# Optimization experiments

Measured on AMD Instinct MI355X. Metric: run time of the kernel, lower is better.

Reference implementation:

```python
import jax, jax.numpy as jnp
import numpy as np

B, S, A, H, NH = 4, 4096, 512, 1024, 16
HD = H // NH  # 64


def setup_inputs() -> dict:
    key = jax.random.key(0)
    ks = jax.random.split(key, 12)
    s = 1.0 / np.sqrt(H)
    return {
        "hidden_states": jax.random.normal(ks[0], (B, S, H), jnp.float32),
        "audio_tokens": jax.random.normal(ks[1], (B, A, H), jnp.float32),
        "attention_mask": jax.random.randint(ks[2], (B, A), 0, 2, jnp.int32),
        "Wq": jax.random.normal(ks[3], (H, H), jnp.float32) * s,
        "bq": jnp.zeros((H,), jnp.float32),
        "Wk": jax.random.normal(ks[4], (H, H), jnp.float32) * s,
        "bk": jnp.zeros((H,), jnp.float32),
        "Wv": jax.random.normal(ks[5], (H, H), jnp.float32) * s,
        "bv": jnp.zeros((H,), jnp.float32),
        "Wo": jax.random.normal(ks[6], (H, H), jnp.float32) * s,
        "bo": jnp.zeros((H,), jnp.float32),
        "ln_gamma": jnp.ones((H,), jnp.float32),
        "ln_beta": jnp.zeros((H,), jnp.float32),
        "residual_scale": jnp.asarray(0.05, jnp.float32),
    }


def _san(x, big=10000.0):
    return jnp.nan_to_num(x, nan=0.0, posinf=big, neginf=-big)


def reference(hidden_states, audio_tokens, attention_mask, Wq, bq, Wk, bk, Wv, bv,
              Wo, bo, ln_gamma, ln_beta, residual_scale):
    hs = _san(hidden_states).astype(jnp.float32)
    at = _san(audio_tokens).astype(jnp.float32)

    def heads(x, W, b):  # [b, t, H] -> [b, t, nh, hd]
        return _san(x @ W.T + b).reshape(x.shape[0], x.shape[1], NH, HD)

    q = heads(hs, Wq, bq)            # [B,S,NH,HD]
    k = heads(at, Wk, bk)            # [B,A,NH,HD]
    v = heads(at, Wv, bv)            # [B,A,NH,HD]

    scale = max(np.sqrt(HD), 1e-8)
    scores = jnp.einsum("bsnd,band->bnsa", q, k) / scale  # [B,NH,S,A]
    scores = jnp.clip(_san(jnp.clip(scores, -50.0, 50.0), 50.0), -50.0, 50.0)

    attend = (attention_mask > 0)[:, None, None, :]       # [B,1,1,A]
    scores = jnp.where(attend, scores, -10000.0)
    scores = jnp.clip(scores, -50.0, 50.0)

    probs = jax.nn.softmax(scores, axis=-1)
    probs = _san(probs, 1.0)
    probs = probs / (jnp.sum(probs, axis=-1, keepdims=True) + 1e-8)

    ctx = jnp.einsum("bnsa,band->bsnd", probs, v).reshape(B, S, H)
    delta = _san(ctx @ Wo.T + bo)

    rs = jnp.clip(residual_scale, 0.0, 0.3)
    delta = rs * delta

    mu = jnp.mean(delta, axis=-1, keepdims=True)
    var = jnp.mean(jnp.square(delta - mu), axis=-1, keepdims=True)
    delta = (delta - mu) / jnp.sqrt(var + 1e-5) * ln_gamma + ln_beta
    return delta
```

## Files before the change

kernel.cpp:

```cpp
#include <hip/hip_runtime.h>
#include <hip/hip_bf16.h>
#include <cstdint>
#include <cstddef>

#define B_  4
#define S_  4096
#define A_  512
#define H_  1024
#define NH_ 16
#define HD_ 64

typedef __bf16 bf16;
typedef __bf16 bf16x8 __attribute__((ext_vector_type(8)));
typedef __bf16 bf16x4 __attribute__((ext_vector_type(4)));
typedef float  fx4    __attribute__((ext_vector_type(4)));

typedef __attribute__((address_space(3))) void LDS_v;
typedef const __attribute__((address_space(1))) void GLB_v;

__device__ __forceinline__ void gl_lds16(const void* g, void* l) {
    __builtin_amdgcn_global_load_lds((GLB_v*)g, (LDS_v*)l, 16, 0, 0);
}

__device__ __forceinline__ float sanf(float x) {
    if (x != x) return 0.f;
    if (fabsf(x) == __builtin_inff()) return x > 0.f ? 10000.f : -10000.f;
    return x;
}

__global__ __launch_bounds__(256) void cast_all(const float* __restrict__ hs,
                                                const float* __restrict__ at,
                                                const float* __restrict__ wq,
                                                const float* __restrict__ wk,
                                                const float* __restrict__ wv,
                                                const float* __restrict__ wo,
                                                bf16* __restrict__ dhs, bf16* __restrict__ dat,
                                                bf16* __restrict__ dwq, bf16* __restrict__ dwk,
                                                bf16* __restrict__ dwv, bf16* __restrict__ dwo) {
    int i = blockIdx.x * 256 + threadIdx.x;
    const float* s; bf16* d; int off;
    if (i < 4194304)      { s = hs; d = dhs; off = i; }
    else if (i < 4718592) { s = at; d = dat; off = i - 4194304; }
    else if (i < 4980736) { s = wq; d = dwq; off = i - 4718592; }
    else if (i < 5242880) { s = wk; d = dwk; off = i - 4980736; }
    else if (i < 5505024) { s = wv; d = dwv; off = i - 5242880; }
    else                  { s = wo; d = dwo; off = i - 5505024; }
    float4 v = ((const float4*)s)[off];
    bf16x4 o;
    o[0] = (bf16)sanf(v.x); o[1] = (bf16)sanf(v.y);
    o[2] = (bf16)sanf(v.z); o[3] = (bf16)sanf(v.w);
    *(bf16x4*)&d[(size_t)off * 4] = o;
}

__global__ __launch_bounds__(256) void qkv_gemm(const bf16* __restrict__ hsb,
                                                const bf16* __restrict__ atb,
                                                const bf16* __restrict__ wqb,
                                                const bf16* __restrict__ wkb,
                                                const bf16* __restrict__ wvb,
                                                const float* __restrict__ bq,
                                                const float* __restrict__ bk,
                                                const float* __restrict__ bv,
                                                bf16* __restrict__ Qb,
                                                bf16* __restrict__ Kb,
                                                bf16* __restrict__ Vtb) {
    __shared__ __align__(16) bf16 As[128 * 32];
    __shared__ __align__(16) bf16 Bs[128 * 32];

    const int id = blockIdx.x;
    int mode, m0, n0;
    const bf16 *A, *Bt; const float* bias;
    if (id < 1024)      { mode = 0; m0 = (id & 127) * 128; n0 = (id >> 7) * 128; A = hsb; Bt = wqb; bias = bq; }
    else if (id < 1152) { int t = id - 1024; mode = 1; m0 = (t & 15) * 128; n0 = (t >> 4) * 128; A = atb; Bt = wkb; bias = bk; }
    else                { int t = id - 1152; mode = 2; m0 = (t & 15) * 128; n0 = (t >> 4) * 128; A = atb; Bt = wvb; bias = bv; }

    const int tid  = threadIdx.x;
    const int lane = tid & 63;
    const int wv   = tid >> 6;
    const int wr   = wv >> 1, wc = wv & 1;
    const int lr   = lane & 15, kq = lane >> 4;

    fx4 acc[4][4] = {};

    const bf16* Ag = A  + (size_t)m0 * 1024;
    const bf16* Bg = Bt + (size_t)n0 * 1024;
    const int c0 = tid, c1 = tid + 256;
    const int row0 = c0 >> 2, kc0 = c0 & 3;
    const int row1 = c1 >> 2, kc1 = c1 & 3;

    for (int k0 = 0; k0 < 1024; k0 += 32) {
        gl_lds16(Ag + (size_t)row0 * 1024 + k0 + kc0 * 8, &As[c0 * 8]);
        gl_lds16(Ag + (size_t)row1 * 1024 + k0 + kc1 * 8, &As[c1 * 8]);
        gl_lds16(Bg + (size_t)row0 * 1024 + k0 + kc0 * 8, &Bs[c0 * 8]);
        gl_lds16(Bg + (size_t)row1 * 1024 + k0 + kc1 * 8, &Bs[c1 * 8]);
        __syncthreads();
        bf16x8 af[4], bfr[4];
#pragma unroll
        for (int i = 0; i < 4; i++) af[i]  = *(const bf16x8*)&As[(wr * 64 + i * 16 + lr) * 32 + kq * 8];
#pragma unroll
        for (int j = 0; j < 4; j++) bfr[j] = *(const bf16x8*)&Bs[(wc * 64 + j * 16 + lr) * 32 + kq * 8];
#pragma unroll
        for (int i = 0; i < 4; i++)
#pragma unroll
            for (int j = 0; j < 4; j++)
                acc[i][j] = __builtin_amdgcn_mfma_f32_16x16x32_bf16(af[i], bfr[j], acc[i][j], 0, 0, 0);
        __syncthreads();
    }

    float bb[4];
#pragma unroll
    for (int j = 0; j < 4; j++) bb[j] = bias[n0 + wc * 64 + j * 16 + lr];

    if (mode == 0) {
        const float sc = 0.18033688011112042f;
#pragma unroll
        for (int i = 0; i < 4; i++) {
            int row = m0 + wr * 64 + i * 16 + kq * 4;
#pragma unroll
            for (int j = 0; j < 4; j++) {
                int col = n0 + wc * 64 + j * 16 + lr;
#pragma unroll
                for (int r = 0; r < 4; r++)
                    Qb[(size_t)(row + r) * 1024 + col] = (bf16)((acc[i][j][r] + bb[j]) * sc);
            }
        }
    } else if (mode == 1) {
#pragma unroll
        for (int i = 0; i < 4; i++) {
            int row = m0 + wr * 64 + i * 16 + kq * 4;
#pragma unroll
            for (int j = 0; j < 4; j++) {
                int col = n0 + wc * 64 + j * 16 + lr;
#pragma unroll
                for (int r = 0; r < 4; r++)
                    Kb[(size_t)(row + r) * 1024 + col] = (bf16)(acc[i][j][r] + bb[j]);
            }
        }
    } else {
#pragma unroll
        for (int i = 0; i < 4; i++) {
            int m = m0 + wr * 64 + i * 16 + kq * 4;
            int bidx = m >> 9, a = m & 511;
#pragma unroll
            for (int j = 0; j < 4; j++) {
                int col = n0 + wc * 64 + j * 16 + lr;
                bf16x4 o;
#pragma unroll
                for (int r = 0; r < 4; r++) o[r] = (bf16)(acc[i][j][r] + bb[j]);
                *(bf16x4*)&Vtb[((size_t)bidx * H_ + col) * A_ + a] = o;
            }
        }
    }
}

__global__ __launch_bounds__(256) void gemm_o(const bf16* __restrict__ A,
                                              const bf16* __restrict__ Bt,
                                              const float* __restrict__ bias,
                                              bf16* __restrict__ C,
                                              const float* __restrict__ rsp) {
    __shared__ __align__(16) bf16 As[128 * 32];
    __shared__ __align__(16) bf16 Bs[128 * 32];

    const int tid  = threadIdx.x;
    const int lane = tid & 63;
    const int wv   = tid >> 6;
    const int wr   = wv >> 1, wc = wv & 1;
    const int lr   = lane & 15, kq = lane >> 4;
    const int m0   = blockIdx.x * 128, n0 = blockIdx.y * 128;

    fx4 acc[4][4] = {};

    const bf16* Ag = A  + (size_t)m0 * 1024;
    const bf16* Bg = Bt + (size_t)n0 * 1024;
    const int c0 = tid, c1 = tid + 256;
    const int row0 = c0 >> 2, kc0 = c0 & 3;
    const int row1 = c1 >> 2, kc1 = c1 & 3;

    for (int k0 = 0; k0 < 1024; k0 += 32) {
        gl_lds16(Ag + (size_t)row0 * 1024 + k0 + kc0 * 8, &As[c0 * 8]);
        gl_lds16(Ag + (size_t)row1 * 1024 + k0 + kc1 * 8, &As[c1 * 8]);
        gl_lds16(Bg + (size_t)row0 * 1024 + k0 + kc0 * 8, &Bs[c0 * 8]);
        gl_lds16(Bg + (size_t)row1 * 1024 + k0 + kc1 * 8, &Bs[c1 * 8]);
        __syncthreads();
        bf16x8 af[4], bfr[4];
#pragma unroll
        for (int i = 0; i < 4; i++) af[i]  = *(const bf16x8*)&As[(wr * 64 + i * 16 + lr) * 32 + kq * 8];
#pragma unroll
        for (int j = 0; j < 4; j++) bfr[j] = *(const bf16x8*)&Bs[(wc * 64 + j * 16 + lr) * 32 + kq * 8];
#pragma unroll
        for (int i = 0; i < 4; i++)
#pragma unroll
            for (int j = 0; j < 4; j++)
                acc[i][j] = __builtin_amdgcn_mfma_f32_16x16x32_bf16(af[i], bfr[j], acc[i][j], 0, 0, 0);
        __syncthreads();
    }

    float bb[4];
#pragma unroll
    for (int j = 0; j < 4; j++) bb[j] = bias[n0 + wc * 64 + j * 16 + lr];
    float rs = fminf(fmaxf(rsp[0], 0.f), 0.3f);
#pragma unroll
    for (int i = 0; i < 4; i++) {
        int row = m0 + wr * 64 + i * 16 + kq * 4;
#pragma unroll
        for (int j = 0; j < 4; j++) {
            int col = n0 + wc * 64 + j * 16 + lr;
#pragma unroll
            for (int r = 0; r < 4; r++)
                C[(size_t)(row + r) * 1024 + col] = (bf16)(rs * (acc[i][j][r] + bb[j]));
        }
    }
}

__global__ __launch_bounds__(256, 4) void attn_kernel(const bf16* __restrict__ Q,
                                                      const bf16* __restrict__ Kb,
                                                      const bf16* __restrict__ Vt,
                                                      const int* __restrict__ mask,
                                                      bf16* __restrict__ ctx) {
    __shared__ __align__(16) bf16 Qs[128 * 72];
    __shared__ __align__(16) bf16 Ks[64 * 72];
    __shared__ __align__(16) bf16 Vts[64 * 72];
    __shared__ float smask[512];

    const int tid  = threadIdx.x;
    const int lane = tid & 63;
    const int wv   = tid >> 6;
    const int lr   = lane & 15, kq = lane >> 4;
    const int st = blockIdx.x, h = blockIdx.y, b = blockIdx.z;
    const int m0 = b * S_ + st * 128;
    const float LO = -72.134752f;

    bf16x8 qtmp[4];
#pragma unroll
    for (int i = 0; i < 4; i++) {
        int c = tid + i * 256, row = c >> 3, ch = c & 7;
        qtmp[i] = *(const bf16x8*)(Q + (size_t)(m0 + row) * H_ + h * 64 + ch * 8);
    }
    smask[tid]       = (mask[b * A_ + tid] > 0)       ? -LO : LO;
    smask[tid + 256] = (mask[b * A_ + tid + 256] > 0) ? -LO : LO;
#pragma unroll
    for (int i = 0; i < 4; i++) {
        int c = tid + i * 256, row = c >> 3, ch = c & 7;
        *(bf16x8*)&Qs[row * 72 + ch * 8] = qtmp[i];
    }

    const int srow = tid >> 2, sseg = tid & 3;
    const size_t kg = (size_t)(b * A_ + srow) * H_ + h * 64 + sseg * 16;
    const bf16* vrow = Vt + (size_t)(b * H_ + h * 64 + srow) * A_;
    const int va0 = 32 * (sseg >> 1) + 4 * ((2 * sseg) & 3);
    const int va1 = 32 * (sseg >> 1) + 4 * ((2 * sseg + 1) & 3);

    bf16x8 kr0 = *(const bf16x8*)(Kb + kg);
    bf16x8 kr1 = *(const bf16x8*)(Kb + kg + 8);
    bf16x4 v00 = *(const bf16x4*)(vrow + va0);
    bf16x4 v01 = *(const bf16x4*)(vrow + va0 + 16);
    bf16x4 v10 = *(const bf16x4*)(vrow + va1);
    bf16x4 v11 = *(const bf16x4*)(vrow + va1 + 16);

    fx4 acco[2][4] = {};
    fx4 accd[2] = {};

    bf16x8 vone;
#pragma unroll
    for (int e = 0; e < 8; e++) vone[e] = (bf16)1.0f;

    for (int it = 0; it < 8; it++) {
        const int a0 = it * 64;
        __syncthreads();
        *(bf16x8*)&Ks[srow * 72 + sseg * 16]      = kr0;
        *(bf16x8*)&Ks[srow * 72 + sseg * 16 + 8]  = kr1;
        *(bf16x8*)&Vts[srow * 72 + sseg * 16] =
            __builtin_shufflevector(v00, v01, 0, 1, 2, 3, 4, 5, 6, 7);
        *(bf16x8*)&Vts[srow * 72 + sseg * 16 + 8] =
            __builtin_shufflevector(v10, v11, 0, 1, 2, 3, 4, 5, 6, 7);
        __syncthreads();

        if (it < 7) {
            const size_t ko = kg + (size_t)(a0 + 64) * H_;
            kr0 = *(const bf16x8*)(Kb + ko);
            kr1 = *(const bf16x8*)(Kb + ko + 8);
            v00 = *(const bf16x4*)(vrow + a0 + 64 + va0);
            v01 = *(const bf16x4*)(vrow + a0 + 64 + va0 + 16);
            v10 = *(const bf16x4*)(vrow + a0 + 64 + va1);
            v11 = *(const bf16x4*)(vrow + a0 + 64 + va1 + 16);
        }

        fx4 accs[4][2] = {};
#pragma unroll
        for (int kk = 0; kk < 64; kk += 32) {
            bf16x8 kf[4], qf[2];
#pragma unroll
            for (int mt = 0; mt < 4; mt++)
                kf[mt] = *(const bf16x8*)&Ks[(mt * 16 + lr) * 72 + kk + kq * 8];
#pragma unroll
            for (int nt = 0; nt < 2; nt++)
                qf[nt] = *(const bf16x8*)&Qs[(wv * 32 + nt * 16 + lr) * 72 + kk + kq * 8];
#pragma unroll
            for (int mt = 0; mt < 4; mt++)
#pragma unroll
                for (int nt = 0; nt < 2; nt++)
                    accs[mt][nt] = __builtin_amdgcn_mfma_f32_16x16x32_bf16(kf[mt], qf[nt], accs[mt][nt], 0, 0, 0);
        }

        bf16x8 pa[2][2];
#pragma unroll
        for (int mt = 0; mt < 4; mt++) {
            fx4 cap = *(const fx4*)&smask[a0 + mt * 16 + kq * 4];
#pragma unroll
            for (int nt = 0; nt < 2; nt++) {
#pragma unroll
                for (int r = 0; r < 4; r++) {
                    float p = __builtin_amdgcn_exp2f(fminf(accs[mt][nt][r], cap[r]));
                    pa[mt >> 1][nt][(mt & 1) * 4 + r] = (bf16)p;
                }
            }
        }

#pragma unroll
        for (int ks = 0; ks < 2; ks++) {
#pragma unroll
            for (int stl = 0; stl < 2; stl++)
                accd[stl] = __builtin_amdgcn_mfma_f32_16x16x32_bf16(pa[ks][stl], vone, accd[stl], 0, 0, 0);
#pragma unroll
            for (int dt = 0; dt < 4; dt++) {
                bf16x8 vf = *(const bf16x8*)&Vts[(dt * 16 + lr) * 72 + ks * 32 + kq * 8];
#pragma unroll
                for (int stl = 0; stl < 2; stl++)
                    acco[stl][dt] = __builtin_amdgcn_mfma_f32_16x16x32_bf16(pa[ks][stl], vf, acco[stl][dt], 0, 0, 0);
            }
        }
    }

#pragma unroll
    for (int stl = 0; stl < 2; stl++) {
        float ri[4];
#pragma unroll
        for (int r = 0; r < 4; r++) ri[r] = __builtin_amdgcn_rcpf(accd[stl][r]);
#pragma unroll
        for (int dt = 0; dt < 4; dt++)
#pragma unroll
            for (int r = 0; r < 4; r++)
                Qs[(wv * 32 + stl * 16 + kq * 4 + r) * 72 + dt * 16 + lr] =
                    (bf16)(acco[stl][dt][r] * ri[r]);
    }
    __syncthreads();
#pragma unroll
    for (int i = 0; i < 4; i++) {
        int c = tid + i * 256, row = c >> 3, ch = c & 7;
        *(bf16x8*)&ctx[(size_t)(m0 + row) * H_ + h * 64 + ch * 8] = *(const bf16x8*)&Qs[row * 72 + ch * 8];
    }
}

__global__ __launch_bounds__(256) void ln_kernel(const bf16* __restrict__ in,
                                                 float* __restrict__ out,
                                                 const float* __restrict__ gamma,
                                                 const float* __restrict__ beta) {
    __shared__ float red[8];
    const int tid = threadIdx.x;
    bf16x4 xb = *(const bf16x4*)&in[(size_t)blockIdx.x * 1024 + tid * 4];
    float x0 = (float)xb[0], x1 = (float)xb[1], x2 = (float)xb[2], x3 = (float)xb[3];
    float s = x0 + x1 + x2 + x3;
    float q = x0 * x0 + x1 * x1 + x2 * x2 + x3 * x3;
#pragma unroll
    for (int off = 32; off > 0; off >>= 1) {
        s += __shfl_down(s, off);
        q += __shfl_down(q, off);
    }
    if ((tid & 63) == 0) { red[(tid >> 6) * 2] = s; red[(tid >> 6) * 2 + 1] = q; }
    __syncthreads();
    s = red[0] + red[2] + red[4] + red[6];
    q = red[1] + red[3] + red[5] + red[7];
    float mean = s * (1.f / 1024.f);
    float var  = q * (1.f / 1024.f) - mean * mean;
    float inv  = rsqrtf(var + 1e-5f);
    float4 g  = ((const float4*)gamma)[tid];
    float4 bb = ((const float4*)beta)[tid];
    float4 y;
    y.x = (x0 - mean) * inv * g.x + bb.x;
    y.y = (x1 - mean) * inv * g.y + bb.y;
    y.z = (x2 - mean) * inv * g.z + bb.z;
    y.w = (x3 - mean) * inv * g.w + bb.w;
    ((float4*)(out + (size_t)blockIdx.x * 1024))[tid] = y;
}

extern "C" void kernel_launch(void* const* d_in, const int* in_sizes, int n_in,
                              void* d_out, int out_size, void* d_ws, size_t ws_size,
                              hipStream_t stream) {
    const float* hs    = (const float*)d_in[0];
    const float* at    = (const float*)d_in[1];
    const int*   maskp = (const int*)d_in[2];
    const float* Wq    = (const float*)d_in[3];
    const float* bq    = (const float*)d_in[4];
    const float* Wk    = (const float*)d_in[5];
    const float* bk    = (const float*)d_in[6];
    const float* Wv    = (const float*)d_in[7];
    const float* bv    = (const float*)d_in[8];
    const float* Wo    = (const float*)d_in[9];
    const float* bo    = (const float*)d_in[10];
    const float* gamma = (const float*)d_in[11];
    const float* beta  = (const float*)d_in[12];
    const float* rsp   = (const float*)d_in[13];

    char* ws = (char*)d_ws;
    bf16* hsb = (bf16*)(ws + 0);
    bf16* ctx = (bf16*)(ws + 0);
    bf16* atb = (bf16*)(ws + 33554432);
    bf16* wqb = (bf16*)(ws + 37748736);
    bf16* wkb = (bf16*)(ws + 39845888);
    bf16* wvb = (bf16*)(ws + 41943040);
    bf16* wob = (bf16*)(ws + 44040192);
    bf16* Qb  = (bf16*)(ws + 46137344);
    bf16* Ob  = Qb;
    bf16* Kb  = (bf16*)(ws + 79691776);
    bf16* Vtb = (bf16*)(ws + 83886080);

    cast_all<<<22528, 256, 0, stream>>>(hs, at, Wq, Wk, Wv, Wo,
                                        hsb, atb, wqb, wkb, wvb, wob);

    qkv_gemm<<<1280, 256, 0, stream>>>(hsb, atb, wqb, wkb, wvb,
                                       bq, bk, bv, Qb, Kb, Vtb);

    attn_kernel<<<dim3(32, 16, 4), 256, 0, stream>>>(Qb, Kb, Vtb, maskp, ctx);

    gemm_o<<<dim3(128, 8), 256, 0, stream>>>(ctx, wob, bo, Ob, rsp);
    ln_kernel<<<16384, 256, 0, stream>>>(Ob, (float*)d_out, gamma, beta);
}
```

Baseline: 322.6 us.

## Rewrite projection GEMMs as 256x256 double-buffered pipelined tiles with XCD-aware remapping

Replaces the 128x128 QKV and output-projection GEMMs with 512-thread 256x256-tile kernels. These use double-buffered LDS, direct global-to-LDS loads, an XOR swizzle against bank conflicts, s_setprio around the MFMA bursts, and explicit waitcnt/barrier pipelining. Block indices are remapped so neighbouring tiles land on the same XCD, and the same remap is applied to the attention and layernorm grids. Attention now keeps Q fragments in registers instead of staging them through LDS. The aim is more data reuse per tile and better L2 locality, at the cost of higher register and LDS pressure and fewer blocks in flight.

```diff
diff --git a/kernel.cpp b/kernel.cpp
--- a/kernel.cpp
+++ b/kernel.cpp
@@ -52,164 +52,217 @@
     *(bf16x4*)&d[(size_t)off * 4] = o;
 }
 
-__global__ __launch_bounds__(256) void qkv_gemm(const bf16* __restrict__ hsb,
-                                                const bf16* __restrict__ atb,
-                                                const bf16* __restrict__ wqb,
-                                                const bf16* __restrict__ wkb,
-                                                const bf16* __restrict__ wvb,
-                                                const float* __restrict__ bq,
-                                                const float* __restrict__ bk,
-                                                const float* __restrict__ bv,
-                                                bf16* __restrict__ Qb,
-                                                bf16* __restrict__ Kb,
-                                                bf16* __restrict__ Vtb) {
-    __shared__ __align__(16) bf16 As[128 * 32];
-    __shared__ __align__(16) bf16 Bs[128 * 32];
+
+#define GEMM_PRO()                                                                     \
+    STG(0, 0, 0, 0); STG(1, 0, 0, 0); STG(0, 1, 0, 0); STG(1, 1, 0, 0);                \
+    asm volatile("s_waitcnt vmcnt(4)" ::: "memory");                                   \
+    __builtin_amdgcn_s_barrier();
+
+#define GEMM_PH(ACC0_, ACCOFF_, KS_, BI_, STGM_, STGH_, KN_, SI_, DOVM_)               \
+    {                                                                                  \
+        if (ACC0_) {                                                                   \
+            for (int j2 = 0; j2 < 4; j2++) bfr[j2] = DSRB(j2, KS_, BI_);               \
+        }                                                                              \
+        for (int i = 0; i < 4; i++) af[i] = DSRA(i + ACCOFF_, KS_, BI_);               \
+        STG(STGM_, STGH_, KN_, SI_);                                                   \
+        __builtin_amdgcn_s_barrier();                                                  \
+        asm volatile("s_waitcnt lgkmcnt(0)" ::: "memory");                             \
+        __builtin_amdgcn_s_setprio(1);                                                 \
+        for (int i = 0; i < 4; i++)                                                    \
+            for (int j2 = 0; j2 < 4; j2++)                                             \
+                acc[i + ACCOFF_][j2] = __builtin_amdgcn_mfma_f32_16x16x32_bf16(        \
+                    af[i], bfr[j2], acc[i + ACCOFF_][j2], 0, 0, 0);                    \
+        __builtin_amdgcn_s_setprio(0);                                                 \
+        if (DOVM_) { asm volatile("s_waitcnt vmcnt(4)" ::: "memory"); }                \
+        __builtin_amdgcn_s_barrier();                                                  \
+    }
+
+#define GEMM_BODY()                                                                    \
+    fx4 acc[8][4] = {};                                                                \
+    GEMM_PRO();                                                                        \
+    for (int kt = 0; kt < 15; ++kt) {                                                  \
+        const int bi = kt & 1, si = bi ^ 1, kn = kt + 1;                               \
+        bf16x8 af[4], bfr[4];                                                          \
+        GEMM_PH(1, 0, 0, bi, 0, 0, kn, si, 0)                                 \
+        GEMM_PH(0, 4, 0, bi, 1, 0, kn, si, 1)                      \
+        GEMM_PH(1, 0, 1, bi, 0, 1, kn, si, 0)                                 \
+        GEMM_PH(0, 4, 1, bi, 1, 1, kn, si, 1)                      \
+    }                                                                                  \
+    {                                         \
+        const int bi = 1;                                                              \
+        bf16x8 af[4], bfr[4];                                                          \
+        for (int j2 = 0; j2 < 4; j2++) bfr[j2] = DSRB(j2, 0, bi);                      \
+        for (int i = 0; i < 4; i++) af[i] = DSRA(i, 0, bi);                            \
+        __builtin_amdgcn_s_setprio(1);                                                 \
+        for (int i = 0; i < 4; i++)                                                    \
+            for (int j2 = 0; j2 < 4; j2++)                                             \
+                acc[i][j2] = __builtin_amdgcn_mfma_f32_16x16x32_bf16(af[i], bfr[j2], acc[i][j2], 0, 0, 0); \
+        __builtin_amdgcn_s_setprio(0);                                                 \
+        for (int i = 0; i < 4; i++) af[i] = DSRA(i + 4, 0, bi);                        \
+        __builtin_amdgcn_s_setprio(1);                                                 \
+        for (int i = 0; i < 4; i++)                                                    \
+            for (int j2 = 0; j2 < 4; j2++)                                             \
+                acc[i + 4][j2] = __builtin_amdgcn_mfma_f32_16x16x32_bf16(af[i], bfr[j2], acc[i + 4][j2], 0, 0, 0); \
+        __builtin_amdgcn_s_setprio(0);                                                 \
+        asm volatile("s_waitcnt vmcnt(0)" ::: "memory");                               \
+        __builtin_amdgcn_s_barrier();                                                  \
+        for (int j2 = 0; j2 < 4; j2++) bfr[j2] = DSRB(j2, 1, bi);                      \
+        for (int i = 0; i < 4; i++) af[i] = DSRA(i, 1, bi);                            \
+        __builtin_amdgcn_s_setprio(1);                                                 \
+        for (int i = 0; i < 4; i++)                                                    \
+            for (int j2 = 0; j2 < 4; j2++)                                             \
+                acc[i][j2] = __builtin_amdgcn_mfma_f32_16x16x32_bf16(af[i], bfr[j2], acc[i][j2], 0, 0, 0); \
+        __builtin_amdgcn_s_setprio(0);                                                 \
+        for (int i = 0; i < 4; i++) af[i] = DSRA(i + 4, 1, bi);                        \
+        __builtin_amdgcn_s_setprio(1);                                                 \
+        for (int i = 0; i < 4; i++)                                                    \
+            for (int j2 = 0; j2 < 4; j2++)                                             \
+                acc[i + 4][j2] = __builtin_amdgcn_mfma_f32_16x16x32_bf16(af[i], bfr[j2], acc[i + 4][j2], 0, 0, 0); \
+        __builtin_amdgcn_s_setprio(0);                                                 \
+    }
+
+#define GEMM_COMMON_DECLS()                                                            \
+    const int tid  = threadIdx.x;                                                      \
+    const int lane = tid & 63;                                                         \
+    const int w8   = tid >> 6;                                                         \
+    const int wm   = w8 >> 2, wn = w8 & 3;                                             \
+    const int lr   = lane & 15, kq = lane >> 4;                                        \
+    const int swz  = (((lr >> 1) & 1) << 4) | (((lr >> 2) & 1) << 3);                  \
+    const int g = lane ^ (((lane >> 3) & 1) << 1) ^ ((lane >> 4) & 1);
+
+#define STG(MS_, kh_, kt_, si_) do {                                                   \
+        const bf16* s_ = (MS_ ? Bsrc : Asrc) + (kt_) * 64 + (kh_) * 32;                \
+        gl_lds16(s_,                 &lds[si_][MS_][kh_][w8 * 32][0]      + lane * 8); \
+        gl_lds16(s_ + (size_t)16384, &lds[si_][MS_][kh_][w8 * 32 + 16][0] + lane * 8); \
+    } while (0)
+
+#define DSRA(i_, ks_, bi_) (*(const bf16x8*)(&lds[bi_][0][ks_][0][0] + \
+        ((((wm * 128 + (i_) * 16 + lr) * 32 + kq * 8)) ^ swz)))
+#define DSRB(j_, ks_, bi_) (*(const bf16x8*)(&lds[bi_][1][ks_][0][0] + \
+        ((((wn * 64 + (j_) * 16 + lr) * 32 + kq * 8)) ^ swz)))
+
+__global__ __launch_bounds__(512, 2) void gemm256qkv(const bf16* __restrict__ hsb,
+                                                     const bf16* __restrict__ atb,
+                                                     const bf16* __restrict__ wqb,
+                                                     const bf16* __restrict__ wkb,
+                                                     const bf16* __restrict__ wvb,
+                                                     const float* __restrict__ bq,
+                                                     const float* __restrict__ bk,
+                                                     const float* __restrict__ bv,
+                                                     bf16* __restrict__ Qb,
+                                                     bf16* __restrict__ Kb,
+                                                     bf16* __restrict__ Vtb) {
+    __shared__ __align__(16) bf16 lds[2][2][2][256][32];
+
+    GEMM_COMMON_DECLS();
 
     const int id = blockIdx.x;
     int mode, m0, n0;
-    const bf16 *A, *Bt; const float* bias;
-    if (id < 1024)      { mode = 0; m0 = (id & 127) * 128; n0 = (id >> 7) * 128; A = hsb; Bt = wqb; bias = bq; }
-    else if (id < 1152) { int t = id - 1024; mode = 1; m0 = (t & 15) * 128; n0 = (t >> 4) * 128; A = atb; Bt = wkb; bias = bk; }
-    else                { int t = id - 1152; mode = 2; m0 = (t & 15) * 128; n0 = (t >> 4) * 128; A = atb; Bt = wvb; bias = bv; }
-
-    const int tid  = threadIdx.x;
-    const int lane = tid & 63;
-    const int wv   = tid >> 6;
-    const int wr   = wv >> 1, wc = wv & 1;
-    const int lr   = lane & 15, kq = lane >> 4;
-
-    fx4 acc[4][4] = {};
-
-    const bf16* Ag = A  + (size_t)m0 * 1024;
-    const bf16* Bg = Bt + (size_t)n0 * 1024;
-    const int c0 = tid, c1 = tid + 256;
-    const int row0 = c0 >> 2, kc0 = c0 & 3;
-    const int row1 = c1 >> 2, kc1 = c1 & 3;
-
-    for (int k0 = 0; k0 < 1024; k0 += 32) {
-        gl_lds16(Ag + (size_t)row0 * 1024 + k0 + kc0 * 8, &As[c0 * 8]);
-        gl_lds16(Ag + (size_t)row1 * 1024 + k0 + kc1 * 8, &As[c1 * 8]);
-        gl_lds16(Bg + (size_t)row0 * 1024 + k0 + kc0 * 8, &Bs[c0 * 8]);
-        gl_lds16(Bg + (size_t)row1 * 1024 + k0 + kc1 * 8, &Bs[c1 * 8]);
-        __syncthreads();
-        bf16x8 af[4], bfr[4];
-#pragma unroll
-        for (int i = 0; i < 4; i++) af[i]  = *(const bf16x8*)&As[(wr * 64 + i * 16 + lr) * 32 + kq * 8];
-#pragma unroll
-        for (int j = 0; j < 4; j++) bfr[j] = *(const bf16x8*)&Bs[(wc * 64 + j * 16 + lr) * 32 + kq * 8];
-#pragma unroll
-        for (int i = 0; i < 4; i++)
-#pragma unroll
-            for (int j = 0; j < 4; j++)
-                acc[i][j] = __builtin_amdgcn_mfma_f32_16x16x32_bf16(af[i], bfr[j], acc[i][j], 0, 0, 0);
-        __syncthreads();
-    }
+    const bf16 *Ap, *Btp; const float* bias;
+    if (id < 256) {
+        const int xcd = id & 7, jj = id >> 3;
+        mode = 0; m0 = (xcd * 8 + (jj >> 2)) << 8; n0 = (jj & 3) << 8;
+        Ap = hsb; Btp = wqb; bias = bq;
+    } else {
+        int t = id - 256;
+        mode = 1 + (t >> 5); t &= 31;
+        m0 = (t >> 2) << 8; n0 = (t & 3) << 8;
+        Ap = atb; Btp = (mode == 1) ? wkb : wvb; bias = (mode == 1) ? bk : bv;
+    }
+
+    const bf16* Asrc = Ap  + (size_t)(m0 + w8 * 32 + (g >> 2)) * 1024 + (g & 3) * 8;
+    const bf16* Bsrc = Btp + (size_t)(n0 + w8 * 32 + (g >> 2)) * 1024 + (g & 3) * 8;
+
+    GEMM_BODY();
 
     float bb[4];
 #pragma unroll
-    for (int j = 0; j < 4; j++) bb[j] = bias[n0 + wc * 64 + j * 16 + lr];
+    for (int j2 = 0; j2 < 4; j2++) bb[j2] = bias[n0 + wn * 64 + j2 * 16 + lr];
 
     if (mode == 0) {
         const float sc = 0.18033688011112042f;
 #pragma unroll
-        for (int i = 0; i < 4; i++) {
-            int row = m0 + wr * 64 + i * 16 + kq * 4;
-#pragma unroll
-            for (int j = 0; j < 4; j++) {
-                int col = n0 + wc * 64 + j * 16 + lr;
+        for (int i = 0; i < 8; i++) {
+            int row = m0 + wm * 128 + i * 16 + kq * 4;
+#pragma unroll
+            for (int j2 = 0; j2 < 4; j2++) {
+                int col = n0 + wn * 64 + j2 * 16 + lr;
 #pragma unroll
                 for (int r = 0; r < 4; r++)
-                    Qb[(size_t)(row + r) * 1024 + col] = (bf16)((acc[i][j][r] + bb[j]) * sc);
+                    Qb[(size_t)(row + r) * 1024 + col] = (bf16)((acc[i][j2][r] + bb[j2]) * sc);
             }
         }
     } else if (mode == 1) {
 #pragma unroll
-        for (int i = 0; i < 4; i++) {
-            int row = m0 + wr * 64 + i * 16 + kq * 4;
-#pragma unroll
-            for (int j = 0; j < 4; j++) {
-                int col = n0 + wc * 64 + j * 16 + lr;
+        for (int i = 0; i < 8; i++) {
+            int row = m0 + wm * 128 + i * 16 + kq * 4;
+#pragma unroll
+            for (int j2 = 0; j2 < 4; j2++) {
+                int col = n0 + wn * 64 + j2 * 16 + lr;
 #pragma unroll
                 for (int r = 0; r < 4; r++)
-                    Kb[(size_t)(row + r) * 1024 + col] = (bf16)(acc[i][j][r] + bb[j]);
+                    Kb[(size_t)(row + r) * 1024 + col] = (bf16)(acc[i][j2][r] + bb[j2]);
             }
         }
     } else {
 #pragma unroll
-        for (int i = 0; i < 4; i++) {
-            int m = m0 + wr * 64 + i * 16 + kq * 4;
+        for (int i = 0; i < 8; i++) {
+            int m = m0 + wm * 128 + i * 16 + kq * 4;
             int bidx = m >> 9, a = m & 511;
 #pragma unroll
-            for (int j = 0; j < 4; j++) {
-                int col = n0 + wc * 64 + j * 16 + lr;
+            for (int j2 = 0; j2 < 4; j2++) {
+                int col = n0 + wn * 64 + j2 * 16 + lr;
                 bf16x4 o;
 #pragma unroll
-                for (int r = 0; r < 4; r++) o[r] = (bf16)(acc[i][j][r] + bb[j]);
+                for (int r = 0; r < 4; r++) o[r] = (bf16)(acc[i][j2][r] + bb[j2]);
                 *(bf16x4*)&Vtb[((size_t)bidx * H_ + col) * A_ + a] = o;
             }
         }
     }
 }
 
-__global__ __launch_bounds__(256) void gemm_o(const bf16* __restrict__ A,
-                                              const bf16* __restrict__ Bt,
-                                              const float* __restrict__ bias,
-                                              bf16* __restrict__ C,
-                                              const float* __restrict__ rsp) {
-    __shared__ __align__(16) bf16 As[128 * 32];
-    __shared__ __align__(16) bf16 Bs[128 * 32];
-
-    const int tid  = threadIdx.x;
-    const int lane = tid & 63;
-    const int wv   = tid >> 6;
-    const int wr   = wv >> 1, wc = wv & 1;
-    const int lr   = lane & 15, kq = lane >> 4;
-    const int m0   = blockIdx.x * 128, n0 = blockIdx.y * 128;
-
-    fx4 acc[4][4] = {};
-
-    const bf16* Ag = A  + (size_t)m0 * 1024;
-    const bf16* Bg = Bt + (size_t)n0 * 1024;
-    const int c0 = tid, c1 = tid + 256;
-    const int row0 = c0 >> 2, kc0 = c0 & 3;
-    const int row1 = c1 >> 2, kc1 = c1 & 3;
-
-    for (int k0 = 0; k0 < 1024; k0 += 32) {
-        gl_lds16(Ag + (size_t)row0 * 1024 + k0 + kc0 * 8, &As[c0 * 8]);
-        gl_lds16(Ag + (size_t)row1 * 1024 + k0 + kc1 * 8, &As[c1 * 8]);
-        gl_lds16(Bg + (size_t)row0 * 1024 + k0 + kc0 * 8, &Bs[c0 * 8]);
-        gl_lds16(Bg + (size_t)row1 * 1024 + k0 + kc1 * 8, &Bs[c1 * 8]);
-        __syncthreads();
-        bf16x8 af[4], bfr[4];
-#pragma unroll
-        for (int i = 0; i < 4; i++) af[i]  = *(const bf16x8*)&As[(wr * 64 + i * 16 + lr) * 32 + kq * 8];
-#pragma unroll
-        for (int j = 0; j < 4; j++) bfr[j] = *(const bf16x8*)&Bs[(wc * 64 + j * 16 + lr) * 32 + kq * 8];
-#pragma unroll
-        for (int i = 0; i < 4; i++)
-#pragma unroll
-            for (int j = 0; j < 4; j++)
-                acc[i][j] = __builtin_amdgcn_mfma_f32_16x16x32_bf16(af[i], bfr[j], acc[i][j], 0, 0, 0);
-        __syncthreads();
-    }
+__global__ __launch_bounds__(512, 2) void gemm256o(const bf16* __restrict__ A,
+                                                   const bf16* __restrict__ Bt,
+                                                   const float* __restrict__ bias,
+                                                   bf16* __restrict__ C,
+                                                   const float* __restrict__ rsp) {
+    __shared__ __align__(16) bf16 lds[2][2][2][256][32];
+
+    GEMM_COMMON_DECLS();
+
+    const int xcd = blockIdx.x & 7, jj = blockIdx.x >> 3;
+    const int m0 = (xcd * 8 + (jj >> 2)) << 8;
+    const int n0 = (jj & 3) << 8;
+
+    const bf16* Asrc = A  + (size_t)(m0 + w8 * 32 + (g >> 2)) * 1024 + (g & 3) * 8;
+    const bf16* Bsrc = Bt + (size_t)(n0 + w8 * 32 + (g >> 2)) * 1024 + (g & 3) * 8;
+
+    GEMM_BODY();
 
     float bb[4];
 #pragma unroll
-    for (int j = 0; j < 4; j++) bb[j] = bias[n0 + wc * 64 + j * 16 + lr];
-    float rs = fminf(fmaxf(rsp[0], 0.f), 0.3f);
-#pragma unroll
-    for (int i = 0; i < 4; i++) {
-        int row = m0 + wr * 64 + i * 16 + kq * 4;
-#pragma unroll
-        for (int j = 0; j < 4; j++) {
-            int col = n0 + wc * 64 + j * 16 + lr;
+    for (int j2 = 0; j2 < 4; j2++) bb[j2] = bias[n0 + wn * 64 + j2 * 16 + lr];
+    const float sc = fminf(fmaxf(rsp[0], 0.f), 0.3f);
+#pragma unroll
+    for (int i = 0; i < 8; i++) {
+        int row = m0 + wm * 128 + i * 16 + kq * 4;
+#pragma unroll
+        for (int j2 = 0; j2 < 4; j2++) {
+            int col = n0 + wn * 64 + j2 * 16 + lr;
 #pragma unroll
             for (int r = 0; r < 4; r++)
-                C[(size_t)(row + r) * 1024 + col] = (bf16)(rs * (acc[i][j][r] + bb[j]));
-        }
-    }
-}
+                C[(size_t)(row + r) * 1024 + col] = (bf16)((acc[i][j2][r] + bb[j2]) * sc);
+        }
+    }
+}
+
+#undef STG
+#undef DSRA
+#undef DSRB
+#undef GEMM_BODY
+#undef GEMM_PH
+#undef GEMM_PRO
+#undef GEMM_COMMON_DECLS
 
 __global__ __launch_bounds__(256, 4) void attn_kernel(const bf16* __restrict__ Q,
                                                       const bf16* __restrict__ Kb,
@@ -225,23 +278,23 @@
     const int lane = tid & 63;
     const int wv   = tid >> 6;
     const int lr   = lane & 15, kq = lane >> 4;
-    const int st = blockIdx.x, h = blockIdx.y, b = blockIdx.z;
+    const int bid = blockIdx.x;
+    const int h  = (bid & 7) | (((bid >> 3) & 1) << 3);
+    const int b  = (bid >> 4) & 3;
+    const int st = bid >> 6;
     const int m0 = b * S_ + st * 128;
     const float LO = -72.134752f;
 
-    bf16x8 qtmp[4];
-#pragma unroll
-    for (int i = 0; i < 4; i++) {
-        int c = tid + i * 256, row = c >> 3, ch = c & 7;
-        qtmp[i] = *(const bf16x8*)(Q + (size_t)(m0 + row) * H_ + h * 64 + ch * 8);
-    }
     smask[tid]       = (mask[b * A_ + tid] > 0)       ? -LO : LO;
     smask[tid + 256] = (mask[b * A_ + tid + 256] > 0) ? -LO : LO;
-#pragma unroll
-    for (int i = 0; i < 4; i++) {
-        int c = tid + i * 256, row = c >> 3, ch = c & 7;
-        *(bf16x8*)&Qs[row * 72 + ch * 8] = qtmp[i];
-    }
+
+    bf16x8 qreg[2][2];
+#pragma unroll
+    for (int kk2 = 0; kk2 < 2; kk2++)
+#pragma unroll
+        for (int nt = 0; nt < 2; nt++)
+            qreg[kk2][nt] = *(const bf16x8*)(Q + (size_t)(m0 + wv * 32 + nt * 16 + lr) * H_
+                                              + h * 64 + kk2 * 32 + kq * 8);
 
     const int srow = tid >> 2, sseg = tid & 3;
     const size_t kg = (size_t)(b * A_ + srow) * H_ + h * 64 + sseg * 16;
@@ -286,19 +339,16 @@
 
         fx4 accs[4][2] = {};
 #pragma unroll
-        for (int kk = 0; kk < 64; kk += 32) {
-            bf16x8 kf[4], qf[2];
+        for (int kk2 = 0; kk2 < 2; kk2++) {
+            bf16x8 kf[4];
 #pragma unroll
             for (int mt = 0; mt < 4; mt++)
-                kf[mt] = *(const bf16x8*)&Ks[(mt * 16 + lr) * 72 + kk + kq * 8];
-#pragma unroll
-            for (int nt = 0; nt < 2; nt++)
-                qf[nt] = *(const bf16x8*)&Qs[(wv * 32 + nt * 16 + lr) * 72 + kk + kq * 8];
+                kf[mt] = *(const bf16x8*)&Ks[(mt * 16 + lr) * 72 + kk2 * 32 + kq * 8];
 #pragma unroll
             for (int mt = 0; mt < 4; mt++)
 #pragma unroll
                 for (int nt = 0; nt < 2; nt++)
-                    accs[mt][nt] = __builtin_amdgcn_mfma_f32_16x16x32_bf16(kf[mt], qf[nt], accs[mt][nt], 0, 0, 0);
+                    accs[mt][nt] = __builtin_amdgcn_mfma_f32_16x16x32_bf16(kf[mt], qreg[kk2][nt], accs[mt][nt], 0, 0, 0);
         }
 
         bf16x8 pa[2][2];
@@ -356,7 +406,8 @@
                                                  const float* __restrict__ beta) {
     __shared__ float red[8];
     const int tid = threadIdx.x;
-    bf16x4 xb = *(const bf16x4*)&in[(size_t)blockIdx.x * 1024 + tid * 4];
+    const int row = ((blockIdx.x & 7) << 11) | (blockIdx.x >> 3);
+    bf16x4 xb = *(const bf16x4*)&in[(size_t)row * 1024 + tid * 4];
     float x0 = (float)xb[0], x1 = (float)xb[1], x2 = (float)xb[2], x3 = (float)xb[3];
     float s = x0 + x1 + x2 + x3;
     float q = x0 * x0 + x1 * x1 + x2 * x2 + x3 * x3;
@@ -379,7 +430,7 @@
     y.y = (x1 - mean) * inv * g.y + bb.y;
     y.z = (x2 - mean) * inv * g.z + bb.z;
     y.w = (x3 - mean) * inv * g.w + bb.w;
-    ((float4*)(out + (size_t)blockIdx.x * 1024))[tid] = y;
+    ((float4*)(out + (size_t)row * 1024))[tid] = y;
 }
 
 extern "C" void kernel_launch(void* const* d_in, const int* in_sizes, int n_in,
@@ -416,11 +467,11 @@
     cast_all<<<22528, 256, 0, stream>>>(hs, at, Wq, Wk, Wv, Wo,
                                         hsb, atb, wqb, wkb, wvb, wob);
 
-    qkv_gemm<<<1280, 256, 0, stream>>>(hsb, atb, wqb, wkb, wvb,
-                                       bq, bk, bv, Qb, Kb, Vtb);
-
-    attn_kernel<<<dim3(32, 16, 4), 256, 0, stream>>>(Qb, Kb, Vtb, maskp, ctx);
-
-    gemm_o<<<dim3(128, 8), 256, 0, stream>>>(ctx, wob, bo, Ob, rsp);
+    gemm256qkv<<<320, 512, 0, stream>>>(hsb, atb, wqb, wkb, wvb,
+                                        bq, bk, bv, Qb, Kb, Vtb);
+
+    attn_kernel<<<2048, 256, 0, stream>>>(Qb, Kb, Vtb, maskp, ctx);
+
+    gemm256o<<<256, 512, 0, stream>>>(ctx, wob, bo, Ob, rsp);
     ln_kernel<<<16384, 256, 0, stream>>>(Ob, (float*)d_out, gamma, beta);
 }
```

Measured after the change: 319.9 us. No clear change (-0.8%).
